# Kernel optimization log

Hardware: AMD Instinct MI355X
Metric: run time of the kernel (lower is better)

Reference implementation:

```python
import jax, jax.numpy as jnp
import numpy as np

N = 4096
IN_F = 256
H = 4
D = 64
WIN = 128
HALF = WIN // 2
TAU = 0.5
TOP_K = 32


def setup_inputs() -> dict:
    key = jax.random.key(0)
    ks = jax.random.split(key, 5)
    node_features = jax.random.normal(ks[0], (N, IN_F), dtype=jnp.float32)
    s = 1.0 / np.sqrt(IN_F)
    Wq = jax.random.normal(ks[1], (IN_F, H * D), dtype=jnp.float32) * s
    bq = jax.random.normal(ks[2], (H * D,), dtype=jnp.float32) * 0.01
    Wk = jax.random.normal(ks[3], (IN_F, H * D), dtype=jnp.float32) * s
    bk = jax.random.normal(ks[4], (H * D,), dtype=jnp.float32) * 0.01
    num_nodes_per_graph = jnp.full((8,), 512, dtype=jnp.int32)  # 8 graphs x 512 = N
    return {"node_features": node_features, "Wq": Wq, "bq": bq, "Wk": Wk,
            "bk": bk, "num_nodes_per_graph": num_nodes_per_graph, "num_relation": 1}


def reference(node_features, Wq, bq, Wk, bk, num_nodes_per_graph, num_relation):
    n = node_features.shape[0]
    scale = jnp.sqrt(jnp.asarray(D, node_features.dtype))

    Q = (node_features @ Wq + bq).reshape(n, H, D)
    K = (node_features @ Wk + bk).reshape(n, H, D)

    # segment boundaries (graph.num_nodes.repeat(num_relation) -> cumsum -> searchsorted)
    segment = jnp.tile(num_nodes_per_graph, num_relation)
    cum = jnp.cumsum(segment)
    i = jnp.arange(n)
    pos = jnp.searchsorted(cum, i, side='right')
    seg_start = jnp.where(pos == 0, 0, cum[jnp.maximum(pos - 1, 0)])
    seg_end = cum[jnp.minimum(pos, cum.shape[0] - 1)]

    start = jnp.maximum(seg_start, i - HALF)  # [N]
    end = jnp.minimum(seg_end, i + HALF)      # [N]

    gather_idx = start[:, None] + jnp.arange(WIN)[None, :]
    valid = gather_idx < end[:, None]
    gi = jnp.clip(gather_idx, 0, n - 1)
    Kw = jnp.where(valid[:, :, None, None], K[gi], 0.0)

    # scores over full window incl. zero padding (faithful: original does not mask softmax)
    scores = jnp.einsum('nhd,nmhd->nhm', Q, Kw) / scale / TAU
    attn = jax.nn.softmax(scores, axis=-1).mean(axis=1)

    # scatter attention rows into dense N x N (padded slots add 0)
    output = jnp.zeros((n, n), node_features.dtype).at[i[:, None], gi].add(
        jnp.where(valid, attn, 0.0))

    # gumbel_softmax_top_k(output, tau, hard=self.k) -> hard=True (k truthy)
    g = jax.random.gumbel(jax.random.key(42), output.shape, output.dtype)
    y_soft = jax.nn.softmax((output + g) / TAU, axis=-1)
    topk_idx = jax.lax.top_k(output, TOP_K)[1]                  # [N, TOP_K]
    y_hard = jnp.zeros_like(output).at[i[:, None], topk_idx].set(1.0)
    y = jax.lax.stop_gradient(y_hard - y_soft) + y_soft
    return y
```

## Files before the change

### kernel.cpp

```cpp
#include <hip/hip_runtime.h>

#define NF    256
#define HD    256
#define NH    4
#define DH    64
#define WINS  128
#define HALFW 64
#define TOPK  32
#define GROWS 32

typedef float vfloat4 __attribute__((ext_vector_type(4)));

__device__ __forceinline__ float dpp_add16(float v) {
    int x;
    x = __builtin_amdgcn_update_dpp(0, __float_as_int(v), 0xB1, 0xF, 0xF, true);
    v += __int_as_float(x);
    x = __builtin_amdgcn_update_dpp(0, __float_as_int(v), 0x4E, 0xF, 0xF, true);
    v += __int_as_float(x);
    x = __builtin_amdgcn_update_dpp(0, __float_as_int(v), 0x124, 0xF, 0xF, true);
    v += __int_as_float(x);
    x = __builtin_amdgcn_update_dpp(0, __float_as_int(v), 0x128, 0xF, 0xF, true);
    v += __int_as_float(x);
    return v;
}

__global__ __launch_bounds__(256) void qk_gemm_kernel(
    const float* __restrict__ X,
    const float* __restrict__ Wq, const float* __restrict__ bq,
    const float* __restrict__ Wk, const float* __restrict__ bk,
    float* __restrict__ Qb, float* __restrict__ Kb, int n)
{
    const int t    = threadIdx.x;
    const int wave = t >> 6;
    const int lane = t & 63;
    const bool isK = (blockIdx.y != 0);
    const float* W   = isK ? Wk : Wq;
    const float* bia = isK ? bk : bq;
    float*       Out = isK ? Kb : Qb;

    const int gx = gridDim.x;
    int bswz = blockIdx.x;
    if ((gx & 7) == 0) {
        int chunk = gx >> 3;
        bswz = (blockIdx.x & 7) * chunk + (blockIdx.x >> 3);
    }
    const int r0  = bswz * GROWS + wave * 8;
    const int r0s = __builtin_amdgcn_readfirstlane(r0);
    const float* Xs = X + (size_t)r0s * NF;

    float4 acc[8];
#pragma unroll
    for (int r = 0; r < 8; ++r) acc[r] = make_float4(0.f, 0.f, 0.f, 0.f);

    float4 wA[8], wB[8];
    const float* Wl = W + 4 * lane;

#pragma unroll
    for (int u = 0; u < 8; ++u)
        wA[u] = *(const float4*)(Wl + (size_t)u * HD);

    for (int k = 0; k < NF; k += 16) {
        if (k + 8 < NF) {
#pragma unroll
            for (int u = 0; u < 8; ++u)
                wB[u] = *(const float4*)(Wl + (size_t)(k + 8 + u) * HD);
        }
#pragma unroll
        for (int u = 0; u < 8; ++u) {
#pragma unroll
            for (int r = 0; r < 8; ++r) {
                float xk = Xs[r * NF + k + u];
                acc[r].x += xk * wA[u].x;
                acc[r].y += xk * wA[u].y;
                acc[r].z += xk * wA[u].z;
                acc[r].w += xk * wA[u].w;
            }
        }
        if (k + 16 < NF) {
#pragma unroll
            for (int u = 0; u < 8; ++u)
                wA[u] = *(const float4*)(Wl + (size_t)(k + 16 + u) * HD);
        }
#pragma unroll
        for (int u = 0; u < 8; ++u) {
#pragma unroll
            for (int r = 0; r < 8; ++r) {
                float xk = Xs[r * NF + k + 8 + u];
                acc[r].x += xk * wB[u].x;
                acc[r].y += xk * wB[u].y;
                acc[r].z += xk * wB[u].z;
                acc[r].w += xk * wB[u].w;
            }
        }
    }

    const float4 bv = *(const float4*)(bia + 4 * lane);
#pragma unroll
    for (int r = 0; r < 8; ++r) {
        acc[r].x += bv.x; acc[r].y += bv.y; acc[r].z += bv.z; acc[r].w += bv.w;
        *(float4*)(Out + (size_t)(r0 + r) * HD + 4 * lane) = acc[r];
    }
}

__global__ __launch_bounds__(256) void attn_topk_kernel(
    const float* __restrict__ Q,
    const float* __restrict__ K,
    const int* __restrict__ nnpg, int n_graphs,
    const int* __restrict__ nrel,
    float* __restrict__ out, int n)
{
    const int t    = threadIdx.x;
    const int wave = t >> 6;
    const int lane = t & 63;

    int i = blockIdx.x;
    const int nb = gridDim.x;
    if ((nb & 7) == 0) {
        int chunk = nb >> 3;
        i = (blockIdx.x & 7) * chunk + (blockIdx.x >> 3);
    }

    __shared__ float sc[NH][WINS + 8];
    __shared__ float pr[NH][WINS];
    __shared__ float attnv[WINS];
    __shared__ float slotval[WINS];

    int R = nrel[0];
    int total = n_graphs * R;
    int seg_start = 0, seg_end = n;
    int cum = 0;
    for (int e = 0; e < total; ++e) {
        int sz = nnpg[e % n_graphs];
        int nc = cum + sz;
        if (i < nc) { seg_start = cum; seg_end = nc; break; }
        cum = nc;
    }
    const int start = max(seg_start, i - HALFW);
    const int end   = min(seg_end,   i + HALFW);
    const int win   = end - start;

    const float4 q4 = *(const float4*)(Q + (size_t)i * HD + lane * 4);

#pragma unroll 8
    for (int j = 0; j < 32; ++j) {
        int row = wave + 4 * j;
        float v = 0.f;
        if (row < win) {
            float4 k4 = *(const float4*)(K + (size_t)(start + row) * HD + lane * 4);
            v = q4.x * k4.x + q4.y * k4.y + q4.z * k4.z + q4.w * k4.w;
        }
        v = dpp_add16(v);
        if ((lane & 15) == 0)
            sc[lane >> 4][row] = v * 0.25f;
    }

    vfloat4* orow = (vfloat4*)(out + (size_t)i * n);
    const int n4  = n >> 2;
    const int lo4 = start >> 2;
    const int hi4 = (end - 1) >> 2;
    const vfloat4 z4 = {0.f, 0.f, 0.f, 0.f};
    for (int c4 = t; c4 < n4; c4 += 256) {
        if (c4 >= lo4 && c4 <= hi4) continue;
        __builtin_nontemporal_store(z4, &orow[c4]);
    }
    __syncthreads();

    {
        float v0 = sc[wave][lane], v1 = sc[wave][lane + 64];
        float mx = fmaxf(v0, v1);
#pragma unroll
        for (int off = 32; off > 0; off >>= 1) mx = fmaxf(mx, __shfl_xor(mx, off));
        float e0 = expf(v0 - mx), e1 = expf(v1 - mx);
        float sm = e0 + e1;
#pragma unroll
        for (int off = 32; off > 0; off >>= 1) sm += __shfl_xor(sm, off);
        pr[wave][lane]      = e0 / sm;
        pr[wave][lane + 64] = e1 / sm;
    }
    __syncthreads();

    if (t < WINS) {
        float a = 0.25f * (pr[0][t] + pr[1][t] + pr[2][t] + pr[3][t]);
        attnv[t] = (t < win) ? a : -1.0f;
    }
    __syncthreads();

    if (t < WINS) {
        float v = attnv[t];
        int cnt = 0;
#pragma unroll
        for (int j4 = 0; j4 < WINS / 4; ++j4) {
            float4 a4 = *(const float4*)&attnv[j4 * 4];
            int jb = j4 * 4;
            cnt += (a4.x > v) || (a4.x == v && (jb + 0) < t);
            cnt += (a4.y > v) || (a4.y == v && (jb + 1) < t);
            cnt += (a4.z > v) || (a4.z == v && (jb + 2) < t);
            cnt += (a4.w > v) || (a4.w == v && (jb + 3) < t);
        }
        slotval[t] = (t < win && cnt < TOPK) ? 1.0f : 0.0f;
    }
    __syncthreads();

    {
        int c4 = lo4 + t;
        if (c4 <= hi4) {
            int c = c4 << 2;
            int o0 = c - start, o1 = o0 + 1, o2 = o0 + 2, o3 = o0 + 3;
            vfloat4 v4;
            v4.x = (o0 >= 0 && o0 < WINS) ? slotval[o0] : 0.f;
            v4.y = (o1 >= 0 && o1 < WINS) ? slotval[o1] : 0.f;
            v4.z = (o2 >= 0 && o2 < WINS) ? slotval[o2] : 0.f;
            v4.w = (o3 >= 0 && o3 < WINS) ? slotval[o3] : 0.f;
            __builtin_nontemporal_store(v4, &orow[c4]);
        }
    }
}

extern "C" void kernel_launch(void* const* d_in, const int* in_sizes, int n_in,
                              void* d_out, int out_size, void* d_ws, size_t ws_size,
                              hipStream_t stream)
{
    const float* X  = (const float*)d_in[0];
    const float* Wq = (const float*)d_in[1];
    const float* bq = (const float*)d_in[2];
    const float* Wk = (const float*)d_in[3];
    const float* bk = (const float*)d_in[4];
    const int* nnpg = (const int*)d_in[5];
    const int* nrel = (const int*)d_in[6];

    const int n = in_sizes[0] / NF;
    const int n_graphs = in_sizes[5];

    float* Qb = (float*)d_ws;
    float* Kb = Qb + (size_t)n * HD;
    float* out = (float*)d_out;

    dim3 gg(n / GROWS, 2);
    qk_gemm_kernel<<<gg, 256, 0, stream>>>(X, Wq, bq, Wk, bk, Qb, Kb, n);

    attn_topk_kernel<<<n, 256, 0, stream>>>(Qb, Kb, nnpg, n_graphs, nrel, out, n);
}
```

Measured before the change: 136.0 us.

## Fuse Q projection into attention kernel and process four query rows per block

Computes Q inside the attention kernel with a split-K projection reduced through shared memory, so the Q buffer no longer goes to global memory and back. Each block now handles four consecutive query rows that share one union of K window rows, so K loads are reused across rows. Softmax, top-k and the output writes become per-wave, one row per wave. The GEMM kernel now computes only K, with smaller row tiles. In exchange, Wq is re-read by every attention block and the block count drops by four.

```diff
diff --git a/kernel.cpp b/kernel.cpp
--- a/kernel.cpp
+++ b/kernel.cpp
@@ -7,7 +7,9 @@
 #define WINS  128
 #define HALFW 64
 #define TOPK  32
-#define GROWS 32
+#define GROWS 16
+#define NB    4
+#define UMAX  136
 
 typedef float vfloat4 __attribute__((ext_vector_type(4)));
 
@@ -24,19 +26,14 @@
     return v;
 }
 
-__global__ __launch_bounds__(256) void qk_gemm_kernel(
+__global__ __launch_bounds__(256) void k_gemm_kernel(
     const float* __restrict__ X,
-    const float* __restrict__ Wq, const float* __restrict__ bq,
     const float* __restrict__ Wk, const float* __restrict__ bk,
-    float* __restrict__ Qb, float* __restrict__ Kb, int n)
+    float* __restrict__ Kb, int n)
 {
     const int t    = threadIdx.x;
     const int wave = t >> 6;
     const int lane = t & 63;
-    const bool isK = (blockIdx.y != 0);
-    const float* W   = isK ? Wk : Wq;
-    const float* bia = isK ? bk : bq;
-    float*       Out = isK ? Kb : Qb;
 
     const int gx = gridDim.x;
     int bswz = blockIdx.x;
@@ -44,16 +41,16 @@
         int chunk = gx >> 3;
         bswz = (blockIdx.x & 7) * chunk + (blockIdx.x >> 3);
     }
-    const int r0  = bswz * GROWS + wave * 8;
+    const int r0  = bswz * GROWS + wave * 4;
     const int r0s = __builtin_amdgcn_readfirstlane(r0);
     const float* Xs = X + (size_t)r0s * NF;
 
-    float4 acc[8];
-#pragma unroll
-    for (int r = 0; r < 8; ++r) acc[r] = make_float4(0.f, 0.f, 0.f, 0.f);
+    float4 acc[4];
+#pragma unroll
+    for (int r = 0; r < 4; ++r) acc[r] = make_float4(0.f, 0.f, 0.f, 0.f);
 
     float4 wA[8], wB[8];
-    const float* Wl = W + 4 * lane;
+    const float* Wl = Wk + 4 * lane;
 
 #pragma unroll
     for (int u = 0; u < 8; ++u)
@@ -68,7 +65,7 @@
 #pragma unroll
         for (int u = 0; u < 8; ++u) {
 #pragma unroll
-            for (int r = 0; r < 8; ++r) {
+            for (int r = 0; r < 4; ++r) {
                 float xk = Xs[r * NF + k + u];
                 acc[r].x += xk * wA[u].x;
                 acc[r].y += xk * wA[u].y;
@@ -84,7 +81,7 @@
 #pragma unroll
         for (int u = 0; u < 8; ++u) {
 #pragma unroll
-            for (int r = 0; r < 8; ++r) {
+            for (int r = 0; r < 4; ++r) {
                 float xk = Xs[r * NF + k + 8 + u];
                 acc[r].x += xk * wB[u].x;
                 acc[r].y += xk * wB[u].y;
@@ -94,16 +91,17 @@
         }
     }
 
-    const float4 bv = *(const float4*)(bia + 4 * lane);
-#pragma unroll
-    for (int r = 0; r < 8; ++r) {
+    const float4 bv = *(const float4*)(bk + 4 * lane);
+#pragma unroll
+    for (int r = 0; r < 4; ++r) {
         acc[r].x += bv.x; acc[r].y += bv.y; acc[r].z += bv.z; acc[r].w += bv.w;
-        *(float4*)(Out + (size_t)(r0 + r) * HD + 4 * lane) = acc[r];
+        *(float4*)(Kb + (size_t)(r0 + r) * HD + 4 * lane) = acc[r];
     }
 }
 
 __global__ __launch_bounds__(256) void attn_topk_kernel(
-    const float* __restrict__ Q,
+    const float* __restrict__ X,
+    const float* __restrict__ Wq, const float* __restrict__ bq,
     const float* __restrict__ K,
     const int* __restrict__ nnpg, int n_graphs,
     const int* __restrict__ nrel,
@@ -113,104 +111,181 @@
     const int wave = t >> 6;
     const int lane = t & 63;
 
-    int i = blockIdx.x;
+    int b = blockIdx.x;
     const int nb = gridDim.x;
     if ((nb & 7) == 0) {
         int chunk = nb >> 3;
-        i = (blockIdx.x & 7) * chunk + (blockIdx.x >> 3);
-    }
-
-    __shared__ float sc[NH][WINS + 8];
-    __shared__ float pr[NH][WINS];
-    __shared__ float attnv[WINS];
-    __shared__ float slotval[WINS];
-
-    int R = nrel[0];
-    int total = n_graphs * R;
-    int seg_start = 0, seg_end = n;
-    int cum = 0;
-    for (int e = 0; e < total; ++e) {
-        int sz = nnpg[e % n_graphs];
-        int nc = cum + sz;
-        if (i < nc) { seg_start = cum; seg_end = nc; break; }
-        cum = nc;
-    }
-    const int start = max(seg_start, i - HALFW);
-    const int end   = min(seg_end,   i + HALFW);
-    const int win   = end - start;
-
-    const float4 q4 = *(const float4*)(Q + (size_t)i * HD + lane * 4);
+        b = (blockIdx.x & 7) * chunk + (blockIdx.x >> 3);
+    }
+    const int i0 = b * NB;
+
+    __shared__ union {
+        float4 qp[4][NB][64];
+        struct {
+            float sc[NB][NH][UMAX];
+            float attnv[NB][WINS];
+        } s;
+    } sh;
+    __shared__ float qsh[NB][HD];
+
+    int st[NB], en[NB];
+    {
+        int R = nrel[0];
+        int total = n_graphs * R;
+#pragma unroll
+        for (int nn = 0; nn < NB; ++nn) {
+            int i = i0 + nn, ss = 0, se = n, cum = 0;
+            for (int e = 0; e < total; ++e) {
+                int sz = nnpg[e % n_graphs];
+                int nc = cum + sz;
+                if (i >= cum && i < nc) { ss = cum; se = nc; }
+                cum = nc;
+            }
+            st[nn] = max(ss, i - HALFW);
+            en[nn] = min(se, i + HALFW);
+        }
+    }
+    const int u0 = st[0];
+    const int U  = en[NB - 1] - u0;
+
+    {
+        const int c4 = t & 63;
+        const int ks = t >> 6;
+        const int i0s = __builtin_amdgcn_readfirstlane(i0);
+        const float* Xs = X + (size_t)i0s * NF;
+
+        float4 qp[NB];
+#pragma unroll
+        for (int nn = 0; nn < NB; ++nn) qp[nn] = make_float4(0.f, 0.f, 0.f, 0.f);
+
+        for (int j = 0; j < 64; j += 8) {
+            float4 wv[8];
+#pragma unroll
+            for (int u = 0; u < 8; ++u)
+                wv[u] = *(const float4*)(Wq + (size_t)(ks + 4 * (j + u)) * HD + 4 * c4);
+#pragma unroll
+            for (int u = 0; u < 8; ++u) {
+                int k = ks + 4 * (j + u);
+#pragma unroll
+                for (int nn = 0; nn < NB; ++nn) {
+                    float xk = Xs[nn * NF + k];
+                    qp[nn].x += xk * wv[u].x;
+                    qp[nn].y += xk * wv[u].y;
+                    qp[nn].z += xk * wv[u].z;
+                    qp[nn].w += xk * wv[u].w;
+                }
+            }
+        }
+#pragma unroll
+        for (int nn = 0; nn < NB; ++nn) sh.qp[ks][nn][c4] = qp[nn];
+    }
+    __syncthreads();
+    {
+        const int nn = t >> 6, c4 = t & 63;
+        float4 a = sh.qp[0][nn][c4], b2 = sh.qp[1][nn][c4];
+        float4 c = sh.qp[2][nn][c4], d = sh.qp[3][nn][c4];
+        const float4 bv = *(const float4*)(bq + 4 * c4);
+        float4 q;
+        q.x = a.x + b2.x + c.x + d.x + bv.x;
+        q.y = a.y + b2.y + c.y + d.y + bv.y;
+        q.z = a.z + b2.z + c.z + d.z + bv.z;
+        q.w = a.w + b2.w + c.w + d.w + bv.w;
+        *(float4*)&qsh[nn][4 * c4] = q;
+    }
+    __syncthreads();
+
+    float4 q4[NB];
+#pragma unroll
+    for (int nn = 0; nn < NB; ++nn)
+        q4[nn] = *(const float4*)&qsh[nn][4 * lane];
 
 #pragma unroll 8
-    for (int j = 0; j < 32; ++j) {
-        int row = wave + 4 * j;
-        float v = 0.f;
-        if (row < win) {
-            float4 k4 = *(const float4*)(K + (size_t)(start + row) * HD + lane * 4);
-            v = q4.x * k4.x + q4.y * k4.y + q4.z * k4.z + q4.w * k4.w;
-        }
-        v = dpp_add16(v);
-        if ((lane & 15) == 0)
-            sc[lane >> 4][row] = v * 0.25f;
-    }
-
-    vfloat4* orow = (vfloat4*)(out + (size_t)i * n);
-    const int n4  = n >> 2;
-    const int lo4 = start >> 2;
-    const int hi4 = (end - 1) >> 2;
-    const vfloat4 z4 = {0.f, 0.f, 0.f, 0.f};
-    for (int c4 = t; c4 < n4; c4 += 256) {
-        if (c4 >= lo4 && c4 <= hi4) continue;
-        __builtin_nontemporal_store(z4, &orow[c4]);
+    for (int j = 0; j < 33; ++j) {
+        int r = wave + 4 * j;
+        bool ok = (r < U);
+        float4 k4 = make_float4(0.f, 0.f, 0.f, 0.f);
+        if (ok)
+            k4 = *(const float4*)(K + (size_t)(u0 + r) * HD + 4 * lane);
+#pragma unroll
+        for (int nn = 0; nn < NB; ++nn) {
+            float d = q4[nn].x * k4.x + q4[nn].y * k4.y
+                    + q4[nn].z * k4.z + q4[nn].w * k4.w;
+            d = dpp_add16(d);
+            if (ok && (lane & 15) == 0)
+                sh.s.sc[nn][lane >> 4][r] = d * 0.25f;
+        }
+    }
+
+    {
+        const int nn = wave;
+        vfloat4* orow = (vfloat4*)(out + (size_t)(i0 + nn) * n);
+        const int n4  = n >> 2;
+        const int lo4 = st[nn] >> 2;
+        const int hi4 = (en[nn] - 1) >> 2;
+        const vfloat4 z4 = {0.f, 0.f, 0.f, 0.f};
+        for (int c4 = lane; c4 < n4; c4 += 64) {
+            if (c4 >= lo4 && c4 <= hi4) continue;
+            __builtin_nontemporal_store(z4, &orow[c4]);
+        }
     }
     __syncthreads();
 
     {
-        float v0 = sc[wave][lane], v1 = sc[wave][lane + 64];
-        float mx = fmaxf(v0, v1);
-#pragma unroll
-        for (int off = 32; off > 0; off >>= 1) mx = fmaxf(mx, __shfl_xor(mx, off));
-        float e0 = expf(v0 - mx), e1 = expf(v1 - mx);
-        float sm = e0 + e1;
-#pragma unroll
-        for (int off = 32; off > 0; off >>= 1) sm += __shfl_xor(sm, off);
-        pr[wave][lane]      = e0 / sm;
-        pr[wave][lane + 64] = e1 / sm;
-    }
-    __syncthreads();
-
-    if (t < WINS) {
-        float a = 0.25f * (pr[0][t] + pr[1][t] + pr[2][t] + pr[3][t]);
-        attnv[t] = (t < win) ? a : -1.0f;
-    }
-    __syncthreads();
-
-    if (t < WINS) {
-        float v = attnv[t];
-        int cnt = 0;
+        const int nn  = wave;
+        const int stn = st[nn], enn = en[nn];
+        const int off = stn - u0;
+        const int win = enn - stn;
+
+        float mean0 = 0.f, mean1 = 0.f;
+#pragma unroll
+        for (int h = 0; h < NH; ++h) {
+            float v0 = (lane      < win) ? sh.s.sc[nn][h][off + lane]      : 0.f;
+            float v1 = (lane + 64 < win) ? sh.s.sc[nn][h][off + lane + 64] : 0.f;
+            float mx = fmaxf(v0, v1);
+#pragma unroll
+            for (int o = 32; o > 0; o >>= 1) mx = fmaxf(mx, __shfl_xor(mx, o));
+            float e0 = expf(v0 - mx), e1 = expf(v1 - mx);
+            float sm = e0 + e1;
+#pragma unroll
+            for (int o = 32; o > 0; o >>= 1) sm += __shfl_xor(sm, o);
+            mean0 += e0 / sm;
+            mean1 += e1 / sm;
+        }
+        const float w0v = (lane      < win) ? mean0 * 0.25f : -1.0f;
+        const float w1v = (lane + 64 < win) ? mean1 * 0.25f : -1.0f;
+        sh.s.attnv[nn][lane]      = w0v;
+        sh.s.attnv[nn][lane + 64] = w1v;
+
+        int cnt0 = 0, cnt1 = 0;
+        const int s0 = lane, s1 = lane + 64;
 #pragma unroll
         for (int j4 = 0; j4 < WINS / 4; ++j4) {
-            float4 a4 = *(const float4*)&attnv[j4 * 4];
+            float4 a4 = *(const float4*)&sh.s.attnv[nn][j4 * 4];
             int jb = j4 * 4;
-            cnt += (a4.x > v) || (a4.x == v && (jb + 0) < t);
-            cnt += (a4.y > v) || (a4.y == v && (jb + 1) < t);
-            cnt += (a4.z > v) || (a4.z == v && (jb + 2) < t);
-            cnt += (a4.w > v) || (a4.w == v && (jb + 3) < t);
-        }
-        slotval[t] = (t < win && cnt < TOPK) ? 1.0f : 0.0f;
-    }
-    __syncthreads();
-
-    {
-        int c4 = lo4 + t;
+            cnt0 += (a4.x > w0v) || (a4.x == w0v && (jb + 0) < s0);
+            cnt0 += (a4.y > w0v) || (a4.y == w0v && (jb + 1) < s0);
+            cnt0 += (a4.z > w0v) || (a4.z == w0v && (jb + 2) < s0);
+            cnt0 += (a4.w > w0v) || (a4.w == w0v && (jb + 3) < s0);
+            cnt1 += (a4.x > w1v) || (a4.x == w1v && (jb + 0) < s1);
+            cnt1 += (a4.y > w1v) || (a4.y == w1v && (jb + 1) < s1);
+            cnt1 += (a4.z > w1v) || (a4.z == w1v && (jb + 2) < s1);
+            cnt1 += (a4.w > w1v) || (a4.w == w1v && (jb + 3) < s1);
+        }
+        sh.s.attnv[nn][s0] = (s0 < win && cnt0 < TOPK) ? 1.0f : 0.0f;
+        sh.s.attnv[nn][s1] = (s1 < win && cnt1 < TOPK) ? 1.0f : 0.0f;
+
+        vfloat4* orow = (vfloat4*)(out + (size_t)(i0 + nn) * n);
+        const int lo4 = stn >> 2;
+        const int hi4 = (enn - 1) >> 2;
+        int c4 = lo4 + lane;
         if (c4 <= hi4) {
             int c = c4 << 2;
-            int o0 = c - start, o1 = o0 + 1, o2 = o0 + 2, o3 = o0 + 3;
+            int o0 = c - stn, o1 = o0 + 1, o2 = o0 + 2, o3 = o0 + 3;
             vfloat4 v4;
-            v4.x = (o0 >= 0 && o0 < WINS) ? slotval[o0] : 0.f;
-            v4.y = (o1 >= 0 && o1 < WINS) ? slotval[o1] : 0.f;
-            v4.z = (o2 >= 0 && o2 < WINS) ? slotval[o2] : 0.f;
-            v4.w = (o3 >= 0 && o3 < WINS) ? slotval[o3] : 0.f;
+            v4.x = (o0 >= 0 && o0 < WINS) ? sh.s.attnv[nn][o0] : 0.f;
+            v4.y = (o1 >= 0 && o1 < WINS) ? sh.s.attnv[nn][o1] : 0.f;
+            v4.z = (o2 >= 0 && o2 < WINS) ? sh.s.attnv[nn][o2] : 0.f;
+            v4.w = (o3 >= 0 && o3 < WINS) ? sh.s.attnv[nn][o3] : 0.f;
             __builtin_nontemporal_store(v4, &orow[c4]);
         }
     }
@@ -231,12 +306,11 @@
     const int n = in_sizes[0] / NF;
     const int n_graphs = in_sizes[5];
 
-    float* Qb = (float*)d_ws;
-    float* Kb = Qb + (size_t)n * HD;
+    float* Kb  = (float*)d_ws;
     float* out = (float*)d_out;
 
-    dim3 gg(n / GROWS, 2);
-    qk_gemm_kernel<<<gg, 256, 0, stream>>>(X, Wq, bq, Wk, bk, Qb, Kb, n);
-
-    attn_topk_kernel<<<n, 256, 0, stream>>>(Qb, Kb, nnpg, n_graphs, nrel, out, n);
+    k_gemm_kernel<<<n / GROWS, 256, 0, stream>>>(X, Wk, bk, Kb, n);
+
+    attn_topk_kernel<<<n / NB, 256, 0, stream>>>(X, Wq, bq, Kb, nnpg, n_graphs,
+                                                 nrel, out, n);
 }
```

New measurement: 139.2 us. 1.02x slower.
